# Optimization experiments

Hardware: AMD Instinct MI355X
Metric: run time of the kernel (lower is better)

The kernel has to match this reference:

```python
import jax, jax.numpy as jnp
import numpy as np

D_MODEL = 1024
N_HEADS = 16
D_HEAD = D_MODEL // N_HEADS


def setup_inputs() -> dict:
    key = jax.random.key(0)
    k_x, k_q, k_k, k_v, k_o = jax.random.split(key, 5)
    scale = 1.0 / np.sqrt(D_MODEL)
    return {
        "x": jax.random.normal(k_x, (4, 2048, D_MODEL), dtype=jnp.float32),
        "W_Q": jax.random.normal(k_q, (D_MODEL, D_MODEL), dtype=jnp.float32) * scale,
        "W_K": jax.random.normal(k_k, (D_MODEL, D_MODEL), dtype=jnp.float32) * scale,
        "W_V": jax.random.normal(k_v, (D_MODEL, D_MODEL), dtype=jnp.float32) * scale,
        "W_O": jax.random.normal(k_o, (D_MODEL, D_MODEL), dtype=jnp.float32) * scale,
    }


def _split_heads(t):
    B, T, D = t.shape
    return t.reshape(B, T, N_HEADS, D_HEAD).transpose(0, 2, 1, 3)  # [B,H,T,Dh]


def reference(x, W_Q, W_K, W_V, W_O):
    B, T, D = x.shape
    # nn.Linear(d,d,bias=False): y = x @ W.T
    q = _split_heads(x @ W_Q.T)
    k = _split_heads(x @ W_K.T)
    v = _split_heads(x @ W_V.T)
    scores = jnp.einsum("bhqd,bhkd->bhqk", q, k) / np.sqrt(D_HEAD).astype(np.float32)
    causal = jnp.tril(jnp.ones((T, T), dtype=bool))
    scores = jnp.where(causal[None, None], scores, jnp.finfo(scores.dtype).min)
    attn = jax.nn.softmax(scores, axis=-1)  # dropout p=0.0 -> identity
    head_out = jnp.einsum("bhqk,bhkd->bhqd", attn, v)
    merged = head_out.transpose(0, 2, 1, 3).reshape(B, T, D)
    out = merged @ W_O.T
    return out
```

## Files before the change

### kernel.cpp

```cpp
#include <hip/hip_runtime.h>
#include <hip/hip_bf16.h>
#include <cstdint>
#include <cstddef>

typedef __bf16 bf16;
typedef __bf16 bf16x8 __attribute__((ext_vector_type(8)));
typedef __bf16 bf16x4 __attribute__((ext_vector_type(4)));
typedef __bf16 bf16x2 __attribute__((ext_vector_type(2)));
typedef float  f32x4  __attribute__((ext_vector_type(4)));
typedef float  f32x16 __attribute__((ext_vector_type(16)));
typedef unsigned int u32x2 __attribute__((ext_vector_type(2)));
typedef unsigned int u32x4 __attribute__((ext_vector_type(4)));

constexpr int D_MODEL = 1024;
constexpr int TT      = 2048;
constexpr int NBATCH  = 4;
constexpr int NH      = 16;
constexpr int QKS     = 2048;
constexpr float C2   = 0.125f * 1.44269504088896340736f;
constexpr float M0C2 = 16.0f * C2;

typedef const __attribute__((address_space(1))) unsigned int* gas_ptr;
typedef       __attribute__((address_space(3))) unsigned int* las_ptr;

__device__ __forceinline__ void gload_lds16(const void* g, void* l) {
  __builtin_amdgcn_global_load_lds((gas_ptr)g, (las_ptr)l, 16, 0, 0);
}

__device__ __forceinline__ void permswap(unsigned int& a, unsigned int& b) {
  u32x2 r = __builtin_amdgcn_permlane32_swap(a, b, false, false);
  a = r[0]; b = r[1];
}

__device__ __forceinline__ unsigned int pk2(float a, float b) {
  bf16x2 t; t[0] = (bf16)a; t[1] = (bf16)b;
  return __builtin_bit_cast(unsigned int, t);
}

__global__ void cvtall_kernel(const float* __restrict__ x,  const float* __restrict__ wq,
                              const float* __restrict__ wk, const float* __restrict__ wv,
                              const float* __restrict__ wo,
                              bf16* __restrict__ xb,  bf16* __restrict__ wqk,
                              bf16* __restrict__ wvb, bf16* __restrict__ wob) {
  const int i = blockIdx.x * 256 + threadIdx.x;
  const float* s; bf16* o; int k;
  if (i < (1 << 21)) {
    s = x; o = xb; k = i;
  } else {
    const int j = i - (1 << 21);
    const int g = j >> 18;
    k = j & ((1 << 18) - 1);
    s = (g == 0) ? wq : (g == 1) ? wk : (g == 2) ? wv : wo;
    o = (g == 0) ? wqk : (g == 1) ? (wqk + (1u << 20)) : (g == 2) ? wvb : wob;
  }
  f32x4 v = reinterpret_cast<const f32x4*>(s)[k];
  bf16x4 t;
  t[0] = (bf16)v[0]; t[1] = (bf16)v[1]; t[2] = (bf16)v[2]; t[3] = (bf16)v[3];
  reinterpret_cast<bf16x4*>(o)[k] = t;
}

template<int OM>
__global__ void gemm_nt(const bf16* __restrict__ A, const bf16* __restrict__ B,
                        void* __restrict__ C, int N) {
  constexpr int KD = 1024;
  __shared__ __align__(16) bf16 At[128 * 32];
  __shared__ __align__(16) bf16 Bt[128 * 32];

  const int tid = threadIdx.x;
  const int w  = tid >> 6, l = tid & 63;
  const int lr = l & 15,  lh = l >> 4;
  const int wr = w >> 1,  wc = w & 1;
  const long brow = (long)blockIdx.x * 128;
  const long bcol = (long)blockIdx.y * 128;

  const int seg_r = l >> 2;
  const int seg_c = (l & 3) * 8;

  f32x4 acc[4][4] = {};

  for (int kk = 0; kk < KD; kk += 32) {
    __syncthreads();
    #pragma unroll
    for (int i = 0; i < 2; ++i) {
      const int seg = w * 2 + i;
      const int row = seg * 16 + seg_r;
      gload_lds16(A + (brow + row) * KD + kk + seg_c, At + seg * 512);
      gload_lds16(B + (bcol + row) * KD + kk + seg_c, Bt + seg * 512);
    }
    __syncthreads();

    bf16x8 af[4], bfr[4];
    #pragma unroll
    for (int m = 0; m < 4; ++m)
      af[m] = *reinterpret_cast<const bf16x8*>(At + (wr * 64 + m * 16 + lr) * 32 + lh * 8);
    #pragma unroll
    for (int n = 0; n < 4; ++n)
      bfr[n] = *reinterpret_cast<const bf16x8*>(Bt + (wc * 64 + n * 16 + lr) * 32 + lh * 8);
    #pragma unroll
    for (int m = 0; m < 4; ++m)
      #pragma unroll
      for (int n = 0; n < 4; ++n)
        acc[m][n] = __builtin_amdgcn_mfma_f32_16x16x32_bf16(af[m], bfr[n], acc[m][n], 0, 0, 0);
  }

  #pragma unroll
  for (int m = 0; m < 4; ++m) {
    #pragma unroll
    for (int n = 0; n < 4; ++n) {
      #pragma unroll
      for (int j = 0; j < 4; ++j) {
        const long gr = brow + wr * 64 + m * 16 + lh * 4 + j;
        const long gc = bcol + wc * 64 + n * 16 + lr;
        const float v = acc[m][n][j];
        if constexpr (OM == 1) ((float*)C)[gr * (long)N + gc] = v;
        else                   ((bf16*)C)[gr * (long)N + gc] = (bf16)v;
      }
    }
  }
}

__global__ __launch_bounds__(256, 3)
void flash_kernel(const bf16* __restrict__ QK, const bf16* __restrict__ Vt,
                  bf16* __restrict__ Om) {
  const int bh  = blockIdx.x;
  const int qt  = 15 - blockIdx.y;
  const int b   = bh >> 4, h = bh & 15;
  const int tid = threadIdx.x;
  const int w   = tid >> 6, l = tid & 63;
  const int l31 = l & 31;
  const int h5  = l >> 5;

  __shared__ __align__(16) bf16 Kl[2][64 * 64];
  __shared__ __align__(16) bf16 Vl[2][64 * 64];

  bf16x8 qf[4];
  {
    const bf16* qp = QK + ((long)(b * TT + qt * 128 + w * 32 + l31)) * QKS + h * 64 + h5 * 8;
    #pragma unroll
    for (int k16 = 0; k16 < 4; ++k16)
      qf[k16] = *reinterpret_cast<const bf16x8*>(qp + k16 * 16);
  }

  f32x16 acc[2] = {};
  float  lp = 0.f;

  int koff[2][4], voff[4][2];
  #pragma unroll
  for (int kb = 0; kb < 2; ++kb) {
    const int row = kb * 32 + l31;
    #pragma unroll
    for (int k16 = 0; k16 < 4; ++k16)
      koff[kb][k16] = row * 128 + ((k16 * 32 + h5 * 16) ^ ((row & 7) << 4));
  }
  #pragma unroll
  for (int db = 0; db < 2; ++db) {
    const int row = db * 32 + l31;
    #pragma unroll
    for (int k4 = 0; k4 < 4; ++k4)
      voff[k4][db] = row * 128 + ((k4 * 32 + h5 * 16) ^ ((row & 7) << 4));
  }

  auto stage = [&](int kt, int p) {
    #pragma unroll
    for (int i = 0; i < 2; ++i) {
      const int ch = i * 256 + w * 64 + l;
      const int r  = ch >> 3;
      const int c  = (ch & 7) ^ (r & 7);
      gload_lds16(QK + ((long)(b * TT + kt * 64 + r)) * QKS + 1024 + h * 64 + c * 8,
                  (bf16*)Kl[p] + (i * 4 + w) * 512);
      gload_lds16(Vt + ((long)(h * 64 + r)) * (NBATCH * TT) + b * TT + kt * 64 + c * 8,
                  (bf16*)Vl[p] + (i * 4 + w) * 512);
    }
  };

  const int NT = 2 * qt + 2;
  stage(0, 0);
  __syncthreads();
  int cur = 0;

  const int wq0 = qt * 128 + w * 32;
  const int qrow = wq0 + l31;

  for (int kt = 0; kt < NT; ++kt) {
    if (kt + 1 < NT) stage(kt + 1, cur ^ 1);

    const char* kbase = (const char*)Kl[cur];
    const char* vbase = (const char*)Vl[cur];

    if (kt * 64 <= wq0 + 31) {
      const bool diag = (kt * 64 + 63 > wq0);

      bf16x8 kf[2][4];
      #pragma unroll
      for (int kb = 0; kb < 2; ++kb)
        #pragma unroll
        for (int k16 = 0; k16 < 4; ++k16)
          kf[kb][k16] = *reinterpret_cast<const bf16x8*>(kbase + koff[kb][k16]);

      f32x16 s[2] = {};
      #pragma unroll
      for (int kb = 0; kb < 2; ++kb)
        #pragma unroll
        for (int k16 = 0; k16 < 4; ++k16)
          s[kb] = __builtin_amdgcn_mfma_f32_32x32x16_bf16(kf[kb][k16], qf[k16], s[kb], 0, 0, 0);

      float lsum = 0.f;
      unsigned int W[2][8];
      #pragma unroll
      for (int kb = 0; kb < 2; ++kb) {
        #pragma unroll
        for (int pr = 0; pr < 8; ++pr) {
          const int r0 = 2 * pr;
          float p0 = __builtin_exp2f(C2 * s[kb][r0]     - M0C2);
          float p1 = __builtin_exp2f(C2 * s[kb][r0 + 1] - M0C2);
          if (diag) {
            const int kv0 = kt * 64 + kb * 32 + (r0 & 3) + 8 * (r0 >> 2) + 4 * h5;
            if (kv0     > qrow) p0 = 0.f;
            if (kv0 + 1 > qrow) p1 = 0.f;
          }
          lsum += p0 + p1;
          W[kb][pr] = pk2(p0, p1);
        }
      }
      lp += lsum;

      bf16x8 vf[4][2];
      #pragma unroll
      for (int k4 = 0; k4 < 4; ++k4)
        #pragma unroll
        for (int db = 0; db < 2; ++db)
          vf[k4][db] = *reinterpret_cast<const bf16x8*>(vbase + voff[k4][db]);

      #pragma unroll
      for (int k4 = 0; k4 < 4; ++k4) {
        const int kb = k4 >> 1, u = (k4 & 1) * 4;
        unsigned int a0 = W[kb][u + 0], b0 = W[kb][u + 2];
        unsigned int a1 = W[kb][u + 1], b1 = W[kb][u + 3];
        permswap(a0, b0);
        permswap(a1, b1);
        u32x4 paw; paw[0] = a0; paw[1] = a1; paw[2] = b0; paw[3] = b1;
        const bf16x8 pa = __builtin_bit_cast(bf16x8, paw);
        #pragma unroll
        for (int db = 0; db < 2; ++db)
          acc[db] = __builtin_amdgcn_mfma_f32_32x32x16_bf16(pa, vf[k4][db], acc[db], 0, 0, 0);
      }
    }

    __syncthreads();
    cur ^= 1;
  }

  {
    float v = lp;
    v += __shfl_xor(v, 32, 64);
    const float li = 1.0f / v;
    #pragma unroll
    for (int r = 0; r < 16; ++r) {
      const int qloc = (r & 3) + 8 * (r >> 2) + 4 * h5;
      const float liw = __shfl(li, qloc, 64);
      const long row = (long)(b * TT + qt * 128 + w * 32 + qloc);
      #pragma unroll
      for (int db = 0; db < 2; ++db)
        Om[row * D_MODEL + h * 64 + db * 32 + l31] = (bf16)(acc[db][r] * liw);
    }
  }
}

extern "C" void kernel_launch(void* const* d_in, const int* in_sizes, int n_in,
                              void* d_out, int out_size, void* d_ws, size_t ws_size,
                              hipStream_t stream) {
  (void)in_sizes; (void)n_in; (void)out_size; (void)ws_size;
  const float* x  = (const float*)d_in[0];
  const float* Wq = (const float*)d_in[1];
  const float* Wk = (const float*)d_in[2];
  const float* Wv = (const float*)d_in[3];
  const float* Wo = (const float*)d_in[4];

  char* ws = (char*)d_ws;
  bf16* xb  = (bf16*)(ws);
  bf16* Wqk = (bf16*)(ws + (16u << 20));
  bf16* Wvb = (bf16*)(ws + (20u << 20));
  bf16* Wob = (bf16*)(ws + (22u << 20));
  bf16* Vt  = (bf16*)(ws + (24u << 20));
  bf16* Mrg = (bf16*)(ws + (40u << 20));
  bf16* QKb = (bf16*)d_out;

  cvtall_kernel<<<(3u << 20) / 256 * 1, 256, 0, stream>>>(x, Wq, Wk, Wv, Wo,
                                                          xb, Wqk, Wvb, Wob);

  gemm_nt<0><<<dim3(64, 16), 256, 0, stream>>>(xb, Wqk, QKb, 2048);
  gemm_nt<0><<<dim3(8, 64), 256, 0, stream>>>(Wvb, xb, Vt, 8192);

  flash_kernel<<<dim3(NBATCH * NH, 16), 256, 0, stream>>>(QKb, Vt, Mrg);

  gemm_nt<1><<<dim3(64, 8), 256, 0, stream>>>(Mrg, Wob, d_out, 1024);
}
```

Baseline: 184.0 us.

## Double GEMM K-tile to 64 with XOR-swizzled LDS layout and launch bounds

The projection GEMM now loads 64-wide K slices per iteration instead of 32. This halves the number of barrier pairs and gives the MFMA loop two sub-steps per load. The LDS tiles are stored with an XOR swizzle on 16-byte chunks keyed by row, which is meant to avoid bank conflicts on the fragment reads. Launch bounds of 3 blocks per SM are added. The cost is doubled LDS per block (32 KB), which may limit occupancy, and there is still no load/compute overlap.

```diff
diff --git a/kernel.cpp b/kernel.cpp
--- a/kernel.cpp
+++ b/kernel.cpp
@@ -55,16 +55,18 @@
   }
   f32x4 v = reinterpret_cast<const f32x4*>(s)[k];
   bf16x4 t;
-  t[0] = (bf16)v[0]; t[1] = (bf16)v[1]; t[2] = (bf16)v[2]; t[3] = (bf16)v[3];
+  t[0] = (bf16)v[0]; t[1] = (bf16)v[1];
+  t[2] = (bf16)v[2]; t[3] = (bf16)v[3];
   reinterpret_cast<bf16x4*>(o)[k] = t;
 }
 
 template<int OM>
-__global__ void gemm_nt(const bf16* __restrict__ A, const bf16* __restrict__ B,
-                        void* __restrict__ C, int N) {
+__global__ __launch_bounds__(256, 3)
+void gemm_nt(const bf16* __restrict__ A, const bf16* __restrict__ B,
+             void* __restrict__ C, int N) {
   constexpr int KD = 1024;
-  __shared__ __align__(16) bf16 At[128 * 32];
-  __shared__ __align__(16) bf16 Bt[128 * 32];
+  __shared__ __align__(16) bf16 At[128 * 64];
+  __shared__ __align__(16) bf16 Bt[128 * 64];
 
   const int tid = threadIdx.x;
   const int w  = tid >> 6, l = tid & 63;
@@ -73,34 +75,41 @@
   const long brow = (long)blockIdx.x * 128;
   const long bcol = (long)blockIdx.y * 128;
 
-  const int seg_r = l >> 2;
-  const int seg_c = (l & 3) * 8;
-
   f32x4 acc[4][4] = {};
 
-  for (int kk = 0; kk < KD; kk += 32) {
+  for (int kk = 0; kk < KD; kk += 64) {
     __syncthreads();
     #pragma unroll
-    for (int i = 0; i < 2; ++i) {
-      const int seg = w * 2 + i;
-      const int row = seg * 16 + seg_r;
-      gload_lds16(A + (brow + row) * KD + kk + seg_c, At + seg * 512);
-      gload_lds16(B + (bcol + row) * KD + kk + seg_c, Bt + seg * 512);
+    for (int j = 0; j < 4; ++j) {
+      const int ch  = j * 256 + w * 64 + l;
+      const int row = ch >> 3;
+      const int c8  = (ch & 7) ^ (row & 7);
+      gload_lds16(A + (brow + row) * KD + kk + c8 * 8, At + (j * 4 + w) * 512);
+      gload_lds16(B + (bcol + row) * KD + kk + c8 * 8, Bt + (j * 4 + w) * 512);
     }
     __syncthreads();
 
-    bf16x8 af[4], bfr[4];
-    #pragma unroll
-    for (int m = 0; m < 4; ++m)
-      af[m] = *reinterpret_cast<const bf16x8*>(At + (wr * 64 + m * 16 + lr) * 32 + lh * 8);
-    #pragma unroll
-    for (int n = 0; n < 4; ++n)
-      bfr[n] = *reinterpret_cast<const bf16x8*>(Bt + (wc * 64 + n * 16 + lr) * 32 + lh * 8);
-    #pragma unroll
-    for (int m = 0; m < 4; ++m)
-      #pragma unroll
-      for (int n = 0; n < 4; ++n)
-        acc[m][n] = __builtin_amdgcn_mfma_f32_16x16x32_bf16(af[m], bfr[n], acc[m][n], 0, 0, 0);
+    #pragma unroll
+    for (int s = 0; s < 2; ++s) {
+      bf16x8 af[4], bfr[4];
+      #pragma unroll
+      for (int m = 0; m < 4; ++m) {
+        const int row = wr * 64 + m * 16 + lr;
+        af[m] = *reinterpret_cast<const bf16x8*>(
+            (const char*)At + row * 128 + ((s * 64 + lh * 16) ^ ((row & 7) << 4)));
+      }
+      #pragma unroll
+      for (int n = 0; n < 4; ++n) {
+        const int row = wc * 64 + n * 16 + lr;
+        bfr[n] = *reinterpret_cast<const bf16x8*>(
+            (const char*)Bt + row * 128 + ((s * 64 + lh * 16) ^ ((row & 7) << 4)));
+      }
+      #pragma unroll
+      for (int m = 0; m < 4; ++m)
+        #pragma unroll
+        for (int n = 0; n < 4; ++n)
+          acc[m][n] = __builtin_amdgcn_mfma_f32_16x16x32_bf16(af[m], bfr[n], acc[m][n], 0, 0, 0);
+    }
   }
 
   #pragma unroll
```

Result: faster. 171.1 us (-7.0%).
